# Performance work log

Measured on AMD Instinct MI355X. Metric: run time of the kernel, lower is better.

Reference implementation:

```python
import jax, jax.numpy as jnp
import numpy as np

NUM_ITERATIONS = 3


def squash(t, axis=-1):
    sn = jnp.sum(t * t, axis=axis, keepdims=True)
    scale = sn / (1.0 + sn)
    return scale * t / jnp.sqrt(sn)


def setup_inputs() -> dict:
    key = jax.random.key(0)
    k1, k2 = jax.random.split(key)
    B, Cin, R = 64, 8, 800
    NC, O = 128, 16
    x = jax.random.normal(k1, (B, Cin, R), dtype=jnp.float32)
    route_weights = jax.random.normal(k2, (NC, R, Cin, O), dtype=jnp.float32)
    return {"x": x, "route_weights": route_weights}


def reference(x, route_weights):
    # x: [B, Cin, R] -> transpose(1,2) -> [B, R, Cin]
    xt = jnp.transpose(x, (0, 2, 1))
    # priors = x[None,:,:,None,:] @ W[:,None] -> [NC, B, R, 1, O]; we drop the
    # singleton dim and keep [NC, B, R, O] (math identical).
    priors = jnp.einsum('bri,crio->cbro', xt, route_weights)
    logits = jnp.zeros_like(priors)
    outputs = None
    for i in range(NUM_ITERATIONS):
        # original custom softmax over dim=2 (route nodes)
        probs = jax.nn.softmax(logits, axis=2)
        outputs = squash(jnp.sum(probs * priors, axis=2, keepdims=True), axis=-1)  # [NC,B,1,O]
        if i != NUM_ITERATIONS - 1:
            delta = jnp.sum(priors * outputs, axis=-1, keepdims=True)  # [NC,B,R,1]
            logits = logits + delta  # broadcast over O, as in torch
    out = jnp.squeeze(outputs, axis=2)          # [NC, B, O]  (squeeze of [NC,B,1,1,O])
    out = jnp.transpose(out, (1, 0, 2))          # [B, NC, O]  (transpose(0,1))
    out = jnp.transpose(out, (0, 2, 1))          # [B, O, NC]  (final transpose(1,2))
    return out
```

## Files before the change

kernel.cpp:

```cpp
#include <hip/hip_runtime.h>
#include <math.h>

namespace {

constexpr int kB   = 64;
constexpr int kCin = 8;
constexpr int kR   = 800;
constexpr int kNC  = 128;
constexpr int kO   = 16;
constexpr int CT   = 256;
constexpr int MT   = 512;
constexpr int NITER = 3;
constexpr size_t WS_NEEDED =
    (size_t)kNC * kO * kR * kCin * sizeof(unsigned short);

typedef _Float16 half2v __attribute__((ext_vector_type(2)));

__device__ __forceinline__ half2v u2h(unsigned int u) {
  union { unsigned int u; half2v h; } x;
  x.u = u;
  return x.h;
}

__device__ __forceinline__ unsigned short f2h(float f) {
  union { _Float16 h; unsigned short s; } x;
  x.h = (_Float16)f;
  return x.s;
}

__device__ __forceinline__ float dpp_xor1_add(float v) {
  const int o = __builtin_amdgcn_mov_dpp(__float_as_int(v), 0xB1, 0xF, 0xF, true);
  return v + __int_as_float(o);
}
__device__ __forceinline__ float dpp_xor2_add(float v) {
  const int o = __builtin_amdgcn_mov_dpp(__float_as_int(v), 0x4E, 0xF, 0xF, true);
  return v + __int_as_float(o);
}
__device__ __forceinline__ float dpp_mir8_add(float v) {
  const int o = __builtin_amdgcn_mov_dpp(__float_as_int(v), 0x141, 0xF, 0xF, true);
  return v + __int_as_float(o);
}

__global__ __launch_bounds__(CT) void conv_w(const float* __restrict__ W,
                                             unsigned short* __restrict__ Wb) {
  __shared__ float tile[32 * 132];
  const int blk = blockIdx.x;
  const int c  = blk / 25;
  const int rt = blk - c * 25;
  const int r0 = rt * 32;
  const int t  = threadIdx.x;

  const float4* src =
      reinterpret_cast<const float4*>(W + ((size_t)c * kR + r0) * kCin * kO);
  #pragma unroll
  for (int k2 = 0; k2 < 4; ++k2) {
    const int i4  = t + k2 * CT;
    const float4 v = src[i4];
    const int fi = i4 * 4, row = fi >> 7, pos = fi & 127;
    *reinterpret_cast<float4*>(&tile[row * 132 + pos]) = v;
  }
  __syncthreads();

  const int o = t >> 4;
  #pragma unroll
  for (int k2 = 0; k2 < 2; ++k2) {
    const int rl = (t & 15) + 16 * k2;
    unsigned int pk[4];
    #pragma unroll
    for (int q = 0; q < 4; ++q) {
      const unsigned int lo = f2h(tile[rl * 132 + (2 * q + 0) * 16 + o]);
      const unsigned int hi = f2h(tile[rl * 132 + (2 * q + 1) * 16 + o]);
      pk[q] = lo | (hi << 16);
    }
    reinterpret_cast<uint4*>(Wb)[(size_t)(c * kO + o) * kR + (r0 + rl)] =
        make_uint4(pk[0], pk[1], pk[2], pk[3]);
  }
}

__global__ __launch_bounds__(MT, 4) void caps_route(
    const float* __restrict__ x, const unsigned short* __restrict__ Wb,
    float* __restrict__ out) {
  constexpr int RST = 20;
  __shared__ float red[128 * RST];
  __shared__ float shs[RST];

  const int t = threadIdx.x;
  const int j   = blockIdx.x;
  const int xcd = j & 7;
  const int kk  = j >> 3;
  const int c   = ((kk >> 6) << 3) + xcd;
  const int b   = kk & 63;

  const float* xb  = x + (size_t)b * kCin * kR;
  const bool  has2 = (t < kR - MT);
  const int   r1   = t, r2 = MT + t;

  half2v P1[8], P2[8];
  #pragma unroll
  for (int q = 0; q < 8; ++q) P2[q] = half2v{(_Float16)0.f, (_Float16)0.f};

  const uint4* Wc = reinterpret_cast<const uint4*>(Wb) + (size_t)c * kO * kR;

  {
    half2v xp[4];
    #pragma unroll
    for (int q = 0; q < 4; ++q)
      xp[q] = half2v{(_Float16)xb[(2*q) * kR + r1], (_Float16)xb[(2*q+1) * kR + r1]};
    float p[16];
    #pragma unroll
    for (int ob = 0; ob < 2; ++ob) {
      uint4 w[8];
      #pragma unroll
      for (int u = 0; u < 8; ++u) w[u] = Wc[(size_t)(ob * 8 + u) * kR + r1];
      #pragma unroll
      for (int u = 0; u < 8; ++u) {
        float a = __builtin_amdgcn_fdot2(u2h(w[u].x), xp[0], 0.f, false);
        a = __builtin_amdgcn_fdot2(u2h(w[u].y), xp[1], a, false);
        a = __builtin_amdgcn_fdot2(u2h(w[u].z), xp[2], a, false);
        a = __builtin_amdgcn_fdot2(u2h(w[u].w), xp[3], a, false);
        p[ob * 8 + u] = a;
      }
    }
    #pragma unroll
    for (int q = 0; q < 8; ++q)
      P1[q] = half2v{(_Float16)p[2*q], (_Float16)p[2*q+1]};
  }
  if (has2) {
    half2v xp[4];
    #pragma unroll
    for (int q = 0; q < 4; ++q)
      xp[q] = half2v{(_Float16)xb[(2*q) * kR + r2], (_Float16)xb[(2*q+1) * kR + r2]};
    float p[16];
    #pragma unroll
    for (int ob = 0; ob < 2; ++ob) {
      uint4 w[8];
      #pragma unroll
      for (int u = 0; u < 8; ++u) w[u] = Wc[(size_t)(ob * 8 + u) * kR + r2];
      #pragma unroll
      for (int u = 0; u < 8; ++u) {
        float a = __builtin_amdgcn_fdot2(u2h(w[u].x), xp[0], 0.f, false);
        a = __builtin_amdgcn_fdot2(u2h(w[u].y), xp[1], a, false);
        a = __builtin_amdgcn_fdot2(u2h(w[u].z), xp[2], a, false);
        a = __builtin_amdgcn_fdot2(u2h(w[u].w), xp[3], a, false);
        p[ob * 8 + u] = a;
      }
    }
    #pragma unroll
    for (int q = 0; q < 8; ++q)
      P2[q] = half2v{(_Float16)p[2*q], (_Float16)p[2*q+1]};
  }

  float l1 = 0.f, l2 = 0.f;
  #pragma unroll
  for (int it = 0; it < NITER; ++it) {
    const float e1 = (it == 0) ? 1.f : __expf(l1);
    const float e2 = has2 ? ((it == 0) ? 1.f : __expf(l2)) : 0.f;

    float u1[kO], u2[kO];
    #pragma unroll
    for (int q = 0; q < 8; ++q) {
      u1[2*q]   = (float)P1[q].x; u1[2*q+1] = (float)P1[q].y;
      u2[2*q]   = (float)P2[q].x; u2[2*q+1] = (float)P2[q].y;
    }

    float sp[kO + 1];
    sp[kO] = e1 + e2;
    #pragma unroll
    for (int o = 0; o < kO; ++o) sp[o] = e1 * u1[o] + e2 * u2[o];

    #pragma unroll
    for (int v = 0; v <= kO; ++v) {
      sp[v] = dpp_xor1_add(sp[v]);
      sp[v] = dpp_xor2_add(sp[v]);
    }
    if ((t & 3) == 0) {
      float* row = &red[(t >> 2) * RST];
      #pragma unroll
      for (int q = 0; q < 4; ++q)
        *reinterpret_cast<float4*>(row + 4 * q) =
            make_float4(sp[4*q], sp[4*q+1], sp[4*q+2], sp[4*q+3]);
      row[16] = sp[16];
    }
    __syncthreads();

    if (t < 136) {
      const int q = t & 7, col = t >> 3;
      float a = 0.f;
      #pragma unroll
      for (int rr = 0; rr < 16; ++rr) a += red[(rr * 8 + q) * RST + col];
      a = dpp_xor1_add(a);
      a = dpp_xor2_add(a);
      a = dpp_mir8_add(a);
      if (q == 0) shs[col] = a;
    }
    __syncthreads();

    const float Zi = 1.f / shs[kO];
    float ss = 0.f;
    #pragma unroll
    for (int o = 0; o < kO; ++o) ss += shs[o] * shs[o];
    const float sn = ss * Zi * Zi;
    const float g  = Zi * sqrtf(sn) / (1.f + sn);

    if (it < NITER - 1) {
      float d1 = 0.f, d2 = 0.f;
      #pragma unroll
      for (int o = 0; o < kO; ++o) { d1 += u1[o] * shs[o]; d2 += u2[o] * shs[o]; }
      l1 += d1 * g;
      if (has2) l2 += d2 * g;
    } else {
      if (t < kO) out[(size_t)b * kO * kNC + t * kNC + c] = shs[t] * g;
    }
  }
}

__global__ __launch_bounds__(MT, 4) void caps_route_f32(
    const float* __restrict__ x, const float* __restrict__ W,
    float* __restrict__ out) {
  constexpr int RST = 20;
  __shared__ float red[128 * RST];
  __shared__ float shs[RST];

  const int t   = threadIdx.x;
  const int j   = blockIdx.x;
  const int xcd = j & 7;
  const int kk  = j >> 3;
  const int c   = ((kk >> 6) << 3) + xcd;
  const int b   = kk & 63;

  const float* xb  = x + (size_t)b * kCin * kR;
  const bool  has2 = (t < kR - MT);
  const int   r1   = t, r2 = MT + t;

  float P1[kO], P2[kO];
  #pragma unroll
  for (int o = 0; o < kO; ++o) P2[o] = 0.f;
  {
    float xa[kCin];
    #pragma unroll
    for (int i = 0; i < kCin; ++i) xa[i] = xb[i * kR + r1];
    const float* Wc = W + ((size_t)c * kR + r1) * kCin * kO;
    #pragma unroll
    for (int o = 0; o < kO; ++o) {
      float acc = 0.f;
      #pragma unroll
      for (int i = 0; i < kCin; ++i) acc += xa[i] * Wc[i * kO + o];
      P1[o] = acc;
    }
  }
  if (has2) {
    float xa[kCin];
    #pragma unroll
    for (int i = 0; i < kCin; ++i) xa[i] = xb[i * kR + r2];
    const float* Wc = W + ((size_t)c * kR + r2) * kCin * kO;
    #pragma unroll
    for (int o = 0; o < kO; ++o) {
      float acc = 0.f;
      #pragma unroll
      for (int i = 0; i < kCin; ++i) acc += xa[i] * Wc[i * kO + o];
      P2[o] = acc;
    }
  }

  float l1 = 0.f, l2 = 0.f;
  #pragma unroll
  for (int it = 0; it < NITER; ++it) {
    const float e1 = (it == 0) ? 1.f : __expf(l1);
    const float e2 = has2 ? ((it == 0) ? 1.f : __expf(l2)) : 0.f;
    float sp[kO + 1];
    sp[kO] = e1 + e2;
    #pragma unroll
    for (int o = 0; o < kO; ++o) sp[o] = e1 * P1[o] + e2 * P2[o];
    #pragma unroll
    for (int v = 0; v <= kO; ++v) {
      sp[v] = dpp_xor1_add(sp[v]);
      sp[v] = dpp_xor2_add(sp[v]);
    }
    if ((t & 3) == 0) {
      float* row = &red[(t >> 2) * RST];
      #pragma unroll
      for (int q = 0; q < 4; ++q)
        *reinterpret_cast<float4*>(row + 4 * q) =
            make_float4(sp[4*q], sp[4*q+1], sp[4*q+2], sp[4*q+3]);
      row[16] = sp[16];
    }
    __syncthreads();
    if (t < 136) {
      const int q = t & 7, col = t >> 3;
      float a = 0.f;
      #pragma unroll
      for (int rr = 0; rr < 16; ++rr) a += red[(rr * 8 + q) * RST + col];
      a = dpp_xor1_add(a);
      a = dpp_xor2_add(a);
      a = dpp_mir8_add(a);
      if (q == 0) shs[col] = a;
    }
    __syncthreads();
    const float Zi = 1.f / shs[kO];
    float ss = 0.f;
    #pragma unroll
    for (int o = 0; o < kO; ++o) ss += shs[o] * shs[o];
    const float sn = ss * Zi * Zi;
    const float g  = Zi * sqrtf(sn) / (1.f + sn);
    if (it < NITER - 1) {
      float d1 = 0.f, d2 = 0.f;
      #pragma unroll
      for (int o = 0; o < kO; ++o) { d1 += P1[o] * shs[o]; d2 += P2[o] * shs[o]; }
      l1 += d1 * g;
      if (has2) l2 += d2 * g;
    } else {
      if (t < kO) out[(size_t)b * kO * kNC + t * kNC + c] = shs[t] * g;
    }
  }
}

}

extern "C" void kernel_launch(void* const* d_in, const int* in_sizes, int n_in,
                              void* d_out, int out_size, void* d_ws, size_t ws_size,
                              hipStream_t stream) {
  const float* x = (const float*)d_in[0];
  const float* W = (const float*)d_in[1];
  float* out = (float*)d_out;
  (void)in_sizes; (void)n_in; (void)out_size;

  if (ws_size >= WS_NEEDED) {
    unsigned short* Wb = (unsigned short*)d_ws;
    conv_w<<<dim3(kNC * 25), dim3(CT), 0, stream>>>(W, Wb);
    caps_route<<<dim3(kNC * kB), dim3(MT), 0, stream>>>(x, Wb, out);
  } else {
    caps_route_f32<<<dim3(kNC * kB), dim3(MT), 0, stream>>>(x, W, out);
  }
}
```

Baseline: 202.0 us.

## Halve routing block size and process four route rows per thread with fp32 priors

The routing kernel now launches 256 threads per block instead of 512. Each thread computes priors for three or four route rows and keeps them in fp32 registers instead of packed fp16. This is meant to cut the shared-memory reduction size and the barrier and conversion overhead per block, and to raise the instruction-level parallelism in each thread. In exchange it uses more registers per thread, leaves the fourth row's extra work to the first wave only, and lowers the thread count per block. The fp32 fallback kernel keeps 512 threads through a separate constant.

```diff
diff --git a/kernel.cpp b/kernel.cpp
--- a/kernel.cpp
+++ b/kernel.cpp
@@ -9,7 +9,8 @@
 constexpr int kNC  = 128;
 constexpr int kO   = 16;
 constexpr int CT   = 256;
-constexpr int MT   = 512;
+constexpr int MT   = 256;
+constexpr int FT   = 512;
 constexpr int NITER = 3;
 constexpr size_t WS_NEEDED =
     (size_t)kNC * kO * kR * kCin * sizeof(unsigned short);
@@ -81,7 +82,7 @@
     const float* __restrict__ x, const unsigned short* __restrict__ Wb,
     float* __restrict__ out) {
   constexpr int RST = 20;
-  __shared__ float red[128 * RST];
+  __shared__ float red[64 * RST];
   __shared__ float shs[RST];
 
   const int t = threadIdx.x;
@@ -92,81 +93,60 @@
   const int b   = kk & 63;
 
   const float* xb  = x + (size_t)b * kCin * kR;
-  const bool  has2 = (t < kR - MT);
-  const int   r1   = t, r2 = MT + t;
-
-  half2v P1[8], P2[8];
-  #pragma unroll
-  for (int q = 0; q < 8; ++q) P2[q] = half2v{(_Float16)0.f, (_Float16)0.f};
+  const bool  has4 = (t < kR - 3 * MT);
+  const int   r0 = t, r1 = MT + t, r2 = 2 * MT + t, r3 = 3 * MT + t;
 
   const uint4* Wc = reinterpret_cast<const uint4*>(Wb) + (size_t)c * kO * kR;
 
-  {
+  float u0[kO], u1[kO], u2[kO], u3[kO];
+  #pragma unroll
+  for (int o = 0; o < kO; ++o) u3[o] = 0.f;
+
+  auto row_dot = [&](int r, float (&uo)[kO]) {
     half2v xp[4];
     #pragma unroll
     for (int q = 0; q < 4; ++q)
-      xp[q] = half2v{(_Float16)xb[(2*q) * kR + r1], (_Float16)xb[(2*q+1) * kR + r1]};
-    float p[16];
+      xp[q] = half2v{(_Float16)xb[(2*q) * kR + r], (_Float16)xb[(2*q+1) * kR + r]};
     #pragma unroll
     for (int ob = 0; ob < 2; ++ob) {
       uint4 w[8];
       #pragma unroll
-      for (int u = 0; u < 8; ++u) w[u] = Wc[(size_t)(ob * 8 + u) * kR + r1];
+      for (int u = 0; u < 8; ++u) w[u] = Wc[(size_t)(ob * 8 + u) * kR + r];
       #pragma unroll
       for (int u = 0; u < 8; ++u) {
         float a = __builtin_amdgcn_fdot2(u2h(w[u].x), xp[0], 0.f, false);
         a = __builtin_amdgcn_fdot2(u2h(w[u].y), xp[1], a, false);
         a = __builtin_amdgcn_fdot2(u2h(w[u].z), xp[2], a, false);
         a = __builtin_amdgcn_fdot2(u2h(w[u].w), xp[3], a, false);
-        p[ob * 8 + u] = a;
+        uo[ob * 8 + u] = a;
       }
     }
-    #pragma unroll
-    for (int q = 0; q < 8; ++q)
-      P1[q] = half2v{(_Float16)p[2*q], (_Float16)p[2*q+1]};
-  }
-  if (has2) {
-    half2v xp[4];
-    #pragma unroll
-    for (int q = 0; q < 4; ++q)
-      xp[q] = half2v{(_Float16)xb[(2*q) * kR + r2], (_Float16)xb[(2*q+1) * kR + r2]};
-    float p[16];
-    #pragma unroll
-    for (int ob = 0; ob < 2; ++ob) {
-      uint4 w[8];
-      #pragma unroll
-      for (int u = 0; u < 8; ++u) w[u] = Wc[(size_t)(ob * 8 + u) * kR + r2];
-      #pragma unroll
-      for (int u = 0; u < 8; ++u) {
-        float a = __builtin_amdgcn_fdot2(u2h(w[u].x), xp[0], 0.f, false);
-        a = __builtin_amdgcn_fdot2(u2h(w[u].y), xp[1], a, false);
-        a = __builtin_amdgcn_fdot2(u2h(w[u].z), xp[2], a, false);
-        a = __builtin_amdgcn_fdot2(u2h(w[u].w), xp[3], a, false);
-        p[ob * 8 + u] = a;
-      }
-    }
-    #pragma unroll
-    for (int q = 0; q < 8; ++q)
-      P2[q] = half2v{(_Float16)p[2*q], (_Float16)p[2*q+1]};
-  }
-
-  float l1 = 0.f, l2 = 0.f;
+  };
+
+  row_dot(r0, u0);
+  row_dot(r1, u1);
+  row_dot(r2, u2);
+  if (has4) row_dot(r3, u3);
+
+  float l0 = 0.f, l1 = 0.f, l2 = 0.f, l3 = 0.f;
   #pragma unroll
   for (int it = 0; it < NITER; ++it) {
+    const float e0 = (it == 0) ? 1.f : __expf(l0);
     const float e1 = (it == 0) ? 1.f : __expf(l1);
-    const float e2 = has2 ? ((it == 0) ? 1.f : __expf(l2)) : 0.f;
-
-    float u1[kO], u2[kO];
-    #pragma unroll
-    for (int q = 0; q < 8; ++q) {
-      u1[2*q]   = (float)P1[q].x; u1[2*q+1] = (float)P1[q].y;
-      u2[2*q]   = (float)P2[q].x; u2[2*q+1] = (float)P2[q].y;
-    }
+    const float e2 = (it == 0) ? 1.f : __expf(l2);
 
     float sp[kO + 1];
-    sp[kO] = e1 + e2;
-    #pragma unroll
-    for (int o = 0; o < kO; ++o) sp[o] = e1 * u1[o] + e2 * u2[o];
+    sp[kO] = e0 + e1 + e2;
+    #pragma unroll
+    for (int o = 0; o < kO; ++o)
+      sp[o] = e0 * u0[o] + e1 * u1[o] + e2 * u2[o];
+
+    if (t < 64) {
+      const float e3 = has4 ? ((it == 0) ? 1.f : __expf(l3)) : 0.f;
+      #pragma unroll
+      for (int o = 0; o < kO; ++o) sp[o] += e3 * u3[o];
+      sp[kO] += e3;
+    }
 
     #pragma unroll
     for (int v = 0; v <= kO; ++v) {
@@ -187,7 +167,7 @@
       const int q = t & 7, col = t >> 3;
       float a = 0.f;
       #pragma unroll
-      for (int rr = 0; rr < 16; ++rr) a += red[(rr * 8 + q) * RST + col];
+      for (int rr = 0; rr < 8; ++rr) a += red[(rr * 8 + q) * RST + col];
       a = dpp_xor1_add(a);
       a = dpp_xor2_add(a);
       a = dpp_mir8_add(a);
@@ -195,26 +175,40 @@
     }
     __syncthreads();
 
+    float sh[kO];
+    #pragma unroll
+    for (int o = 0; o < kO; ++o) sh[o] = shs[o];
     const float Zi = 1.f / shs[kO];
     float ss = 0.f;
     #pragma unroll
-    for (int o = 0; o < kO; ++o) ss += shs[o] * shs[o];
+    for (int o = 0; o < kO; ++o) ss += sh[o] * sh[o];
     const float sn = ss * Zi * Zi;
     const float g  = Zi * sqrtf(sn) / (1.f + sn);
 
     if (it < NITER - 1) {
-      float d1 = 0.f, d2 = 0.f;
-      #pragma unroll
-      for (int o = 0; o < kO; ++o) { d1 += u1[o] * shs[o]; d2 += u2[o] * shs[o]; }
+      float d0 = 0.f, d1 = 0.f, d2 = 0.f;
+      #pragma unroll
+      for (int o = 0; o < kO; ++o) {
+        d0 += u0[o] * sh[o];
+        d1 += u1[o] * sh[o];
+        d2 += u2[o] * sh[o];
+      }
+      l0 += d0 * g;
       l1 += d1 * g;
-      if (has2) l2 += d2 * g;
+      l2 += d2 * g;
+      if (t < 64) {
+        float d3 = 0.f;
+        #pragma unroll
+        for (int o = 0; o < kO; ++o) d3 += u3[o] * sh[o];
+        if (has4) l3 += d3 * g;
+      }
     } else {
       if (t < kO) out[(size_t)b * kO * kNC + t * kNC + c] = shs[t] * g;
     }
   }
 }
 
-__global__ __launch_bounds__(MT, 4) void caps_route_f32(
+__global__ __launch_bounds__(FT, 4) void caps_route_f32(
     const float* __restrict__ x, const float* __restrict__ W,
     float* __restrict__ out) {
   constexpr int RST = 20;
@@ -229,8 +223,8 @@
   const int b   = kk & 63;
 
   const float* xb  = x + (size_t)b * kCin * kR;
-  const bool  has2 = (t < kR - MT);
-  const int   r1   = t, r2 = MT + t;
+  const bool  has2 = (t < kR - FT);
+  const int   r1   = t, r2 = FT + t;
 
   float P1[kO], P2[kO];
   #pragma unroll
@@ -329,6 +323,6 @@
     conv_w<<<dim3(kNC * 25), dim3(CT), 0, stream>>>(W, Wb);
     caps_route<<<dim3(kNC * kB), dim3(MT), 0, stream>>>(x, Wb, out);
   } else {
-    caps_route_f32<<<dim3(kNC * kB), dim3(MT), 0, stream>>>(x, W, out);
-  }
-}
+    caps_route_f32<<<dim3(kNC * kB), dim3(FT), 0, stream>>>(x, W, out);
+  }
+}
```

Result: slower. 452.6 us (+124.1%).
